# Optimization experiments

Hardware: AMD Instinct MI355X
Metric: run time of the kernel (lower is better)

## Reference

```python
import jax, jax.numpy as jnp
import numpy as np

B, S, H = 2, 1024, 1024
E, I, K = 16, 512, 4
SHARED_I = 512 * 2  # moe_intermediate_size * moe_num_shared_experts
NORM_MIN = 1e-12


def _mlp(x, gw, uw, dw):
    # gated SiLU MLP: down(silu(gate(x)) * up(x))
    return (jax.nn.silu(x @ gw) * (x @ uw)) @ dw


def setup_inputs() -> dict:
    key = jax.random.key(0)
    ks = jax.random.split(key, 9)
    s = 0.02
    return {
        "hidden_states": jax.random.normal(ks[0], (B, S, H), jnp.float32),
        "gate_weight": jax.random.normal(ks[1], (H, E), jnp.float32) * s,
        "corr_bias": jnp.zeros((E,), jnp.float32),
        "gate_w": jax.random.normal(ks[2], (E, H, I), jnp.float32) * s,
        "up_w": jax.random.normal(ks[3], (E, H, I), jnp.float32) * s,
        "down_w": jax.random.normal(ks[4], (E, I, H), jnp.float32) * s,
        "shared_gate_w": jax.random.normal(ks[5], (H, SHARED_I), jnp.float32) * s,
        "shared_up_w": jax.random.normal(ks[6], (H, SHARED_I), jnp.float32) * s,
        "shared_down_w": jax.random.normal(ks[7], (SHARED_I, H), jnp.float32) * s,
    }


def reference(hidden_states, gate_weight, corr_bias, gate_w, up_w, down_w,
              shared_gate_w, shared_up_w, shared_down_w):
    b, s, h = hidden_states.shape
    x = hidden_states.reshape(-1, h)                      # [T, H]
    T = x.shape[0]

    # shared experts (full-capacity, always applied)
    shared_out = _mlp(x, shared_gate_w, shared_up_w, shared_down_w)

    # router in float32
    router_logits = x.astype(jnp.float32) @ gate_weight   # [T, E]
    probs = jax.nn.softmax(router_logits, axis=-1)
    # top-k on bias-corrected scores, weights gathered from uncorrected probs
    _, selected = jax.lax.top_k(probs + corr_bias[None, :], K)  # [T, K]
    rw = jnp.take_along_axis(probs, selected, axis=-1)          # [T, K]
    rw = rw / jnp.maximum(rw.sum(-1, keepdims=True), NORM_MIN)
    rw = rw.astype(x.dtype)

    # dense combine weights [T, E] (zero for unselected experts)
    cw = jnp.zeros((T, gate_weight.shape[1]), x.dtype)
    cw = cw.at[jnp.arange(T)[:, None], selected].add(rw)

    # grouped expert MLPs (full capacity, no token dropping)
    g = jnp.einsum('th,ehi->tei', x, gate_w)
    u = jnp.einsum('th,ehi->tei', x, up_w)
    eo = jnp.einsum('tei,eih->teh', jax.nn.silu(g) * u, down_w)
    final = jnp.einsum('teh,te->th', eo, cw) + shared_out

    return final.reshape(b, s, h), router_logits
```

## Files before the change

kernel.cpp:

```cpp
#include <hip/hip_runtime.h>
#include <hip/hip_bf16.h>

#define T_TOK 2048
#define H_DIM 1024
#define E_NUM 16
#define I_DIM 512
#define K_TOP 4
#define SI_DIM 1024

typedef __bf16 bf16x8 __attribute__((ext_vector_type(8)));
typedef __bf16 bf16x4 __attribute__((ext_vector_type(4)));
typedef float f32x4 __attribute__((ext_vector_type(4)));

#define GL2L(g, l)                                                                       \
  __builtin_amdgcn_global_load_lds((const __attribute__((address_space(1))) void*)(g),   \
                                   (__attribute__((address_space(3))) void*)(l), 16, 0, 0)
#define BAR() __builtin_amdgcn_s_barrier()

__global__ __launch_bounds__(256) void transpose_all_kernel(
    const float* __restrict__ gate_w, const float* __restrict__ up_w,
    const float* __restrict__ down_w, const float* __restrict__ sgw,
    const float* __restrict__ suw, const float* __restrict__ sdw,
    const float* __restrict__ gate_weight, __bf16* __restrict__ gw_t,
    __bf16* __restrict__ uw_t, __bf16* __restrict__ dw_t, __bf16* __restrict__ sgw_t,
    __bf16* __restrict__ suw_t, __bf16* __restrict__ sdw_t, float* __restrict__ gwt_f) {
  int tid = threadIdx.x;
  if (blockIdx.x >= 6912) {
    int b = blockIdx.x - 6912;
#pragma unroll
    for (int k = 0; k < 4; k++) {
      int idx = k * 4096 + b * 256 + tid;
      gwt_f[idx] = gate_weight[(idx & 1023) * E_NUM + (idx >> 10)];
    }
    return;
  }
  __shared__ __align__(16) __bf16 tile[64 * 64];
  int t = blockIdx.x;
  const float* in;
  __bf16* out;
  int R, C, r0, c0;
  if (t < 4096) {
    bool g = t < 2048;
    int b = t & 2047;
    int z = b >> 7;
    int ti = b & 127;
    R = H_DIM;
    C = I_DIM;
    r0 = (ti >> 3) * 64;
    c0 = (ti & 7) * 64;
    size_t off = (size_t)z * R * C;
    in = (g ? gate_w : up_w) + off;
    out = (g ? gw_t : uw_t) + off;
  } else if (t < 6144) {
    int b = t - 4096;
    int z = b >> 7;
    int ti = b & 127;
    R = I_DIM;
    C = H_DIM;
    r0 = (ti >> 4) * 64;
    c0 = (ti & 15) * 64;
    size_t off = (size_t)z * R * C;
    in = down_w + off;
    out = dw_t + off;
  } else {
    int b = t - 6144;
    int m = b >> 8;
    int ti = b & 255;
    R = 1024;
    C = 1024;
    r0 = (ti >> 4) * 64;
    c0 = (ti & 15) * 64;
    in = m == 0 ? sgw : m == 1 ? suw : sdw;
    out = m == 0 ? sgw_t : m == 1 ? suw_t : sdw_t;
  }
#pragma unroll
  for (int q = 0; q < 2; q++) {
    int lin8 = q * 256 + tid;
    int row = lin8 >> 3, cb = lin8 & 7;
    const float* ip = in + (size_t)(r0 + row) * C + c0 + cb * 8;
    float4 v0 = *(const float4*)ip;
    float4 v1 = *(const float4*)(ip + 4);
    bf16x8 o;
    o[0] = (__bf16)v0.x; o[1] = (__bf16)v0.y; o[2] = (__bf16)v0.z; o[3] = (__bf16)v0.w;
    o[4] = (__bf16)v1.x; o[5] = (__bf16)v1.y; o[6] = (__bf16)v1.z; o[7] = (__bf16)v1.w;
    int pcb = cb ^ ((row >> 3) & 7);
    *(bf16x8*)&tile[row * 64 + pcb * 8] = o;
  }
  __syncthreads();
  int p = tid >> 3, seg = tid & 7;
  int c = p * 2;
  const unsigned int* ldsw = (const unsigned int*)tile;
  unsigned int d[8];
#pragma unroll
  for (int i = 0; i < 8; i++) {
    int r = seg * 8 + i;
    int pcb = (p >> 2) ^ seg;
    d[i] = ldsw[r * 32 + pcb * 4 + (p & 3)];
  }
  unsigned int lo[4], hi[4];
#pragma unroll
  for (int j = 0; j < 4; j++) {
    lo[j] = __builtin_amdgcn_perm(d[2 * j + 1], d[2 * j], 0x05040100u);
    hi[j] = __builtin_amdgcn_perm(d[2 * j + 1], d[2 * j], 0x07060302u);
  }
  __bf16* op0 = out + (size_t)(c0 + c) * R + r0 + seg * 8;
  __bf16* op1 = op0 + R;
  *(uint4*)op0 = make_uint4(lo[0], lo[1], lo[2], lo[3]);
  *(uint4*)op1 = make_uint4(hi[0], hi[1], hi[2], hi[3]);
}

__global__ __launch_bounds__(256) void router_kernel(
    const float* __restrict__ x, const float* __restrict__ gwt, const float* __restrict__ cbias,
    float* __restrict__ logits_out, __bf16* __restrict__ x_bf, int* __restrict__ selE,
    float* __restrict__ selW) {
  int t = blockIdx.x;
  int tid = threadIdx.x;
  int wid = tid >> 6, lane = tid & 63;
  int e = lane >> 2, cl = lane & 3;
  int c = wid * 4 + cl;
  const float* xr = x + (size_t)t * H_DIM + c * 64;
  const float* gr = gwt + (size_t)e * H_DIM + c * 64;
  float a0 = 0.f, a1 = 0.f, a2 = 0.f, a3 = 0.f;
#pragma unroll
  for (int j = 0; j < 16; j++) {
    float4 xv = *(const float4*)(xr + j * 4);
    float4 gv = *(const float4*)(gr + j * 4);
    if (e == 0) {
      bf16x4 o = {(__bf16)xv.x, (__bf16)xv.y, (__bf16)xv.z, (__bf16)xv.w};
      *(bf16x4*)(x_bf + (size_t)t * H_DIM + c * 64 + j * 4) = o;
    }
    a0 = fmaf(xv.x, gv.x, a0);
    a1 = fmaf(xv.y, gv.y, a1);
    a2 = fmaf(xv.z, gv.z, a2);
    a3 = fmaf(xv.w, gv.w, a3);
  }
  float a = (a0 + a1) + (a2 + a3);
  a += __shfl_xor(a, 1);
  a += __shfl_xor(a, 2);
  __shared__ float part[4][16];
  if (cl == 0) part[wid][e] = a;
  __syncthreads();
  if (wid != 0) return;
  float logit = -1e30f;
  if (lane < E_NUM)
    logit = (part[0][lane] + part[1][lane]) + (part[2][lane] + part[3][lane]);
  if (lane < E_NUM) logits_out[(size_t)t * E_NUM + lane] = logit;
  float m = logit;
#pragma unroll
  for (int mk = 8; mk >= 1; mk >>= 1) m = fmaxf(m, __shfl_xor(m, mk));
  float p = __expf(logit - m);
  float s = p;
#pragma unroll
  for (int mk = 8; mk >= 1; mk >>= 1) s += __shfl_xor(s, mk);
  p /= s;
  float score = (lane < E_NUM) ? p + cbias[lane] : -1e30f;
  int sel[K_TOP];
  float w[K_TOP];
#pragma unroll
  for (int k = 0; k < K_TOP; k++) {
    float bv = score;
    int bi = (lane < E_NUM) ? lane : 999;
#pragma unroll
    for (int mk = 1; mk <= 8; mk <<= 1) {
      float ov = __shfl_xor(bv, mk);
      int oi = __shfl_xor(bi, mk);
      if (ov > bv || (ov == bv && oi < bi)) {
        bv = ov;
        bi = oi;
      }
    }
    sel[k] = bi;
    w[k] = __shfl(p, bi);
    if (lane == bi) score = -1e30f;
  }
  if (lane == 0) {
    float wsum = fmaxf(w[0] + w[1] + w[2] + w[3], 1e-12f);
#pragma unroll
    for (int k = 0; k < K_TOP; k++) {
      selE[t * K_TOP + k] = sel[k];
      selW[t * K_TOP + k] = w[k] / wsum;
    }
  }
}

__global__ __launch_bounds__(1024) void count_place_kernel(
    const int* __restrict__ selE, int* __restrict__ counts, int* __restrict__ offs,
    int* __restrict__ slot_of_tk, int* __restrict__ tok_of_slot) {
  int tid = threadIdx.x;
  int wv = tid >> 6, lane = tid & 63;
  unsigned long long lt = (1ULL << lane) - 1ULL;
  __shared__ int wcnt[16][16];
  __shared__ int wbase[16][16];
  __shared__ int glob[16];
  __shared__ int offsh[16];
  if (tid < 16) glob[tid] = 0;
  __syncthreads();
  int ex[8], rk[8];
#pragma unroll
  for (int r = 0; r < 8; r++) {
    int e = selE[r * 1024 + tid];
    ex[r] = e;
    int rank = 0;
#pragma unroll
    for (int q = 0; q < 16; q++) {
      unsigned long long b = __ballot(e == q);
      int c = __popcll(b & lt);
      if (e == q) rank = c;
      if (lane == q) wcnt[wv][q] = __popcll(b);
    }
    __syncthreads();
    if (wv == 0 && lane < 16) {
      int run = glob[lane];
#pragma unroll
      for (int w = 0; w < 16; w++) {
        wbase[w][lane] = run;
        run += wcnt[w][lane];
      }
      glob[lane] = run;
    }
    __syncthreads();
    rk[r] = rank + wbase[wv][e];
    __syncthreads();
  }
  if (wv == 0 && lane == 0) {
    int s = 0;
#pragma unroll
    for (int q = 0; q < 16; q++) {
      offsh[q] = s;
      s += glob[q];
    }
  }
  __syncthreads();
  if (tid < 16) {
    counts[tid] = glob[tid];
    offs[tid] = offsh[tid];
  }
#pragma unroll
  for (int r = 0; r < 8; r++) {
    int entry = r * 1024 + tid;
    int slot = offsh[ex[r]] + rk[r];
    slot_of_tk[entry] = slot;
    tok_of_slot[slot] = entry >> 2;
  }
}

__global__ __launch_bounds__(256, 3) void gemm_stage1(
    const __bf16* __restrict__ x_bf, const int* __restrict__ tok_of_slot,
    const int* __restrict__ counts, const int* __restrict__ offs, const __bf16* __restrict__ gw_t,
    const __bf16* __restrict__ uw_t, const __bf16* __restrict__ sgw_t,
    const __bf16* __restrict__ suw_t, __bf16* __restrict__ he, __bf16* __restrict__ hs) {
  __shared__ __align__(16) __bf16 Alds[128 * 64];
  __shared__ __align__(16) __bf16 Bgl[2 * 64 * 64];
  __shared__ __align__(16) __bf16 Bul[2 * 64 * 64];
  int z = blockIdx.z, bx = blockIdx.x, m0 = blockIdx.y * 128;
  const __bf16 *Bg, *Bu;
  __bf16* Cp;
  const int* tokIdx;
  int rowOff, M, ldC, n0;
  if (z < E_NUM) {
    M = counts[z];
    if (m0 >= M) return;
    tokIdx = tok_of_slot;
    rowOff = offs[z];
    Bg = gw_t + (size_t)z * I_DIM * H_DIM;
    Bu = uw_t + (size_t)z * I_DIM * H_DIM;
    Cp = he;
    ldC = I_DIM;
    n0 = bx * 64;
  } else {
    tokIdx = nullptr;
    rowOff = 0;
    M = T_TOK;
    Bg = sgw_t;
    Bu = suw_t;
    Cp = hs;
    ldC = SI_DIM;
    n0 = (z - E_NUM) * 512 + bx * 64;
  }
  int tid = threadIdx.x;
  int wave = tid >> 6, lane = tid & 63;
  int rsub = lane >> 3, chunk = lane & 7;
  int sch = (chunk ^ rsub) * 8;
  size_t aB[4], bB[2];
#pragma unroll
  for (int j = 0; j < 4; j++) {
    int r = wave * 32 + j * 8 + rsub;
    int ar = m0 + r;
    ar = ar < M - 1 ? ar : M - 1;
    int grow = tokIdx ? tokIdx[rowOff + ar] : rowOff + ar;
    aB[j] = (size_t)grow * H_DIM + sch;
  }
#pragma unroll
  for (int j = 0; j < 2; j++) {
    int r = wave * 16 + j * 8 + rsub;
    bB[j] = (size_t)(n0 + r) * H_DIM + sch;
  }
  int wm = (wave >> 1) * 64, wn = (wave & 1) * 32;
  int rl = lane & 15, gq = lane >> 4;
  int xa = rl & 7;

  auto STAGE_A = [&](int k0) {
#pragma unroll
    for (int j = 0; j < 4; j++) GL2L(x_bf + aB[j] + k0, Alds + (wave * 32 + j * 8) * 64);
  };
  auto STAGE_B = [&](int k0, int buf) {
#pragma unroll
    for (int j = 0; j < 2; j++) {
      int ld = buf * 4096 + (wave * 16 + j * 8) * 64;
      GL2L(Bg + bB[j] + k0, Bgl + ld);
      GL2L(Bu + bB[j] + k0, Bul + ld);
    }
  };

  f32x4 accg[4][2] = {}, accu[4][2] = {};
  const int NT = H_DIM / 64;
  STAGE_A(0);
  STAGE_B(0, 0);
  int buf = 0;
  for (int t = 0; t < NT; ++t) {
    if (t + 1 < NT) {
      STAGE_B((t + 1) << 6, buf ^ 1);
      asm volatile("s_waitcnt vmcnt(4)" ::: "memory");
    } else {
      asm volatile("s_waitcnt vmcnt(0)" ::: "memory");
    }
    BAR();
    const __bf16* Bgr = Bgl + buf * 4096;
    const __bf16* Bur = Bul + buf * 4096;
#pragma unroll
    for (int s = 0; s < 2; s++) {
      int lc = ((s * 4 + gq) ^ xa) * 8;
      bf16x8 af[4], bg[2], bu[2];
#pragma unroll
      for (int m = 0; m < 4; m++) af[m] = *(const bf16x8*)&Alds[(wm + m * 16 + rl) * 64 + lc];
#pragma unroll
      for (int n = 0; n < 2; n++) {
        bg[n] = *(const bf16x8*)&Bgr[(wn + n * 16 + rl) * 64 + lc];
        bu[n] = *(const bf16x8*)&Bur[(wn + n * 16 + rl) * 64 + lc];
      }
#pragma unroll
      for (int m = 0; m < 4; m++)
#pragma unroll
        for (int n = 0; n < 2; n++) {
          accg[m][n] =
              __builtin_amdgcn_mfma_f32_16x16x32_bf16(af[m], bg[n], accg[m][n], 0, 0, 0);
          accu[m][n] =
              __builtin_amdgcn_mfma_f32_16x16x32_bf16(af[m], bu[n], accu[m][n], 0, 0, 0);
        }
    }
    BAR();
    if (t + 1 < NT) STAGE_A((t + 1) << 6);
    buf ^= 1;
  }
#pragma unroll
  for (int m = 0; m < 4; m++) {
#pragma unroll
    for (int b = 0; b < 4; b++) {
      int row = m0 + wm + m * 16 + gq * 4 + b;
      if (row < M) {
        size_t rb = (size_t)(rowOff + row) * ldC + n0 + wn + rl;
#pragma unroll
        for (int n = 0; n < 2; n++) {
          float g = accg[m][n][b];
          float u = accu[m][n][b];
          float h = g / (1.f + __expf(-g)) * u;
          Cp[rb + n * 16] = (__bf16)h;
        }
      }
    }
  }
}

__global__ __launch_bounds__(256, 4) void gemm_stage2(
    const __bf16* __restrict__ he, const __bf16* __restrict__ hs, const int* __restrict__ counts,
    const int* __restrict__ offs, const __bf16* __restrict__ dw_t,
    const __bf16* __restrict__ sdw_t, __bf16* __restrict__ eo, __bf16* __restrict__ so) {
  __shared__ __align__(16) __bf16 Alds[64 * 64];
  __shared__ __align__(16) __bf16 Blds[2 * 64 * 64];
  int z = blockIdx.z, bx = blockIdx.x, m0 = blockIdx.y * 64;
  const __bf16 *A, *Bp;
  __bf16* Cp;
  int rowOff, M, K;
  if (z < E_NUM) {
    M = counts[z];
    if (m0 >= M) return;
    A = he;
    rowOff = offs[z];
    K = I_DIM;
    Bp = dw_t + (size_t)z * H_DIM * I_DIM;
    Cp = eo;
  } else {
    A = hs;
    rowOff = 0;
    M = T_TOK;
    K = SI_DIM;
    Bp = sdw_t;
    Cp = so;
  }
  int n0 = bx * 64;
  int tid = threadIdx.x;
  int wave = tid >> 6, lane = tid & 63;
  int rsub = lane >> 3, chunk = lane & 7;
  int sch = (chunk ^ rsub) * 8;
  size_t aB[2], bB[2];
#pragma unroll
  for (int j = 0; j < 2; j++) {
    int r = wave * 16 + j * 8 + rsub;
    int ar = m0 + r;
    ar = ar < M - 1 ? ar : M - 1;
    aB[j] = (size_t)(rowOff + ar) * K + sch;
    bB[j] = (size_t)(n0 + r) * K + sch;
  }
  int wm = (wave >> 1) * 32, wn = (wave & 1) * 32;
  int rl = lane & 15, gq = lane >> 4;
  int xa = rl & 7;

  auto STAGE_A = [&](int k0) {
#pragma unroll
    for (int j = 0; j < 2; j++) GL2L(A + aB[j] + k0, Alds + (wave * 16 + j * 8) * 64);
  };
  auto STAGE_B = [&](int k0, int b) {
#pragma unroll
    for (int j = 0; j < 2; j++)
      GL2L(Bp + bB[j] + k0, Blds + b * 4096 + (wave * 16 + j * 8) * 64);
  };

  f32x4 acc[2][2] = {};
  const int NT = K >> 6;
  STAGE_A(0);
  STAGE_B(0, 0);
  int buf = 0;
  for (int t = 0; t < NT; ++t) {
    if (t + 1 < NT) {
      STAGE_B((t + 1) << 6, buf ^ 1);
      asm volatile("s_waitcnt vmcnt(2)" ::: "memory");
    } else {
      asm volatile("s_waitcnt vmcnt(0)" ::: "memory");
    }
    BAR();
    const __bf16* Br = Blds + buf * 4096;
#pragma unroll
    for (int s = 0; s < 2; s++) {
      int lc = ((s * 4 + gq) ^ xa) * 8;
      bf16x8 af[2], bfr[2];
#pragma unroll
      for (int m = 0; m < 2; m++) af[m] = *(const bf16x8*)&Alds[(wm + m * 16 + rl) * 64 + lc];
#pragma unroll
      for (int n = 0; n < 2; n++) bfr[n] = *(const bf16x8*)&Br[(wn + n * 16 + rl) * 64 + lc];
#pragma unroll
      for (int m = 0; m < 2; m++)
#pragma unroll
        for (int n = 0; n < 2; n++)
          acc[m][n] =
              __builtin_amdgcn_mfma_f32_16x16x32_bf16(af[m], bfr[n], acc[m][n], 0, 0, 0);
    }
    BAR();
    if (t + 1 < NT) STAGE_A((t + 1) << 6);
    buf ^= 1;
  }
#pragma unroll
  for (int m = 0; m < 2; m++) {
#pragma unroll
    for (int b = 0; b < 4; b++) {
      int row = m0 + wm + m * 16 + gq * 4 + b;
      if (row < M) {
        size_t rb = (size_t)(rowOff + row) * H_DIM + n0 + wn + rl;
#pragma unroll
        for (int n = 0; n < 2; n++) Cp[rb + n * 16] = (__bf16)acc[m][n][b];
      }
    }
  }
}

__global__ void combine_kernel(const __bf16* __restrict__ eo, const __bf16* __restrict__ so,
                               const int* __restrict__ slot_of_tk, const float* __restrict__ selW,
                               float* __restrict__ out) {
  int idx = blockIdx.x * blockDim.x + threadIdx.x;
  int t = idx >> 8;
  int h4 = (idx & 255) * 4;
  if (t >= T_TOK) return;
  bf16x4 sv = *(const bf16x4*)(so + (size_t)t * H_DIM + h4);
  float a0 = (float)sv[0], a1 = (float)sv[1], a2 = (float)sv[2], a3 = (float)sv[3];
#pragma unroll
  for (int k = 0; k < K_TOP; k++) {
    int slot = slot_of_tk[t * K_TOP + k];
    float w = selW[t * K_TOP + k];
    bf16x4 ev = *(const bf16x4*)(eo + (size_t)slot * H_DIM + h4);
    a0 += w * (float)ev[0];
    a1 += w * (float)ev[1];
    a2 += w * (float)ev[2];
    a3 += w * (float)ev[3];
  }
  *(float4*)(out + (size_t)t * H_DIM + h4) = make_float4(a0, a1, a2, a3);
}

extern "C" void kernel_launch(void* const* d_in, const int* in_sizes, int n_in, void* d_out,
                              int out_size, void* d_ws, size_t ws_size, hipStream_t stream) {
  const float* x = (const float*)d_in[0];
  const float* gate_weight = (const float*)d_in[1];
  const float* corr_bias = (const float*)d_in[2];
  const float* gate_w = (const float*)d_in[3];
  const float* up_w = (const float*)d_in[4];
  const float* down_w = (const float*)d_in[5];
  const float* sgw = (const float*)d_in[6];
  const float* suw = (const float*)d_in[7];
  const float* sdw = (const float*)d_in[8];
  float* out = (float*)d_out;
  float* logits_out = out + (size_t)T_TOK * H_DIM;

  char* wsb = (char*)d_ws;
  size_t o = 0;
  auto nxt = [&](size_t bytes) -> void* {
    void* p = wsb + o;
    o += (bytes + 1023) & ~(size_t)1023;
    return p;
  };
  const size_t EXP_ELE = (size_t)T_TOK * K_TOP * I_DIM;
  const size_t SH_ELE = (size_t)T_TOK * SI_DIM;
  __bf16* x_bf = (__bf16*)nxt((size_t)T_TOK * H_DIM * 2);
  __bf16* gw_t = (__bf16*)nxt((size_t)E_NUM * I_DIM * H_DIM * 2);
  __bf16* uw_t = (__bf16*)nxt((size_t)E_NUM * I_DIM * H_DIM * 2);
  __bf16* dw_t = (__bf16*)nxt((size_t)E_NUM * H_DIM * I_DIM * 2);
  __bf16* sgw_t = (__bf16*)nxt((size_t)SI_DIM * H_DIM * 2);
  __bf16* suw_t = (__bf16*)nxt((size_t)SI_DIM * H_DIM * 2);
  __bf16* sdw_t = (__bf16*)nxt((size_t)H_DIM * SI_DIM * 2);
  __bf16* h_all = (__bf16*)nxt((EXP_ELE + SH_ELE) * 2);
  __bf16* eo = (__bf16*)nxt((size_t)T_TOK * K_TOP * H_DIM * 2);
  __bf16* so = (__bf16*)nxt((size_t)T_TOK * H_DIM * 2);
  float* gwt_f = (float*)nxt((size_t)E_NUM * H_DIM * 4);
  int* counts = (int*)nxt(64);
  int* offs = (int*)nxt(128);
  int* selE = (int*)nxt((size_t)T_TOK * K_TOP * 4);
  float* selW = (float*)nxt((size_t)T_TOK * K_TOP * 4);
  int* slot_of_tk = (int*)nxt((size_t)T_TOK * K_TOP * 4);
  int* tok_of_slot = (int*)nxt((size_t)T_TOK * K_TOP * 4);
  __bf16* he = h_all;
  __bf16* hs = h_all + EXP_ELE;
  (void)ws_size;
  (void)in_sizes;
  (void)n_in;
  (void)out_size;

  transpose_all_kernel<<<6928, 256, 0, stream>>>(gate_w, up_w, down_w, sgw, suw, sdw,
                                                 gate_weight, gw_t, uw_t, dw_t, sgw_t, suw_t,
                                                 sdw_t, gwt_f);
  router_kernel<<<T_TOK, 256, 0, stream>>>(x, gwt_f, corr_bias, logits_out, x_bf, selE, selW);
  count_place_kernel<<<1, 1024, 0, stream>>>(selE, counts, offs, slot_of_tk, tok_of_slot);

  gemm_stage1<<<dim3(8, 16, E_NUM + 2), 256, 0, stream>>>(x_bf, tok_of_slot, counts, offs, gw_t,
                                                          uw_t, sgw_t, suw_t, he, hs);
  gemm_stage2<<<dim3(16, 32, E_NUM + 1), 256, 0, stream>>>(he, hs, counts, offs, dw_t, sdw_t, eo,
                                                           so);

  combine_kernel<<<(T_TOK * H_DIM / 4) / 256, 256, 0, stream>>>(eo, so, slot_of_tk, selW, out);
}
```

Measured before the change: 154.6 us.

## Restructure router so each wavefront handles two tokens without LDS reduction

The router kernel now assigns two tokens to each wavefront and eight tokens to each block. Each lane covers one expert over a quarter of the hidden dimension, and partial sums are reduced with cross-lane shuffles, which removes the shared-memory partial buffer and the block barrier. The intent is to cut block count, barrier cost and idle waves in the softmax/top-k tail. In exchange, each lane runs a longer serial loop with strided per-lane loads that coalesce less well, and there are only 256 blocks to cover the GPU.

New measurement: 160.7 us. +4.0%, slower.

```diff
diff --git a/kernel.cpp b/kernel.cpp
--- a/kernel.cpp
+++ b/kernel.cpp
@@ -113,72 +113,68 @@
     const float* __restrict__ x, const float* __restrict__ gwt, const float* __restrict__ cbias,
     float* __restrict__ logits_out, __bf16* __restrict__ x_bf, int* __restrict__ selE,
     float* __restrict__ selW) {
-  int t = blockIdx.x;
   int tid = threadIdx.x;
   int wid = tid >> 6, lane = tid & 63;
-  int e = lane >> 2, cl = lane & 3;
-  int c = wid * 4 + cl;
-  const float* xr = x + (size_t)t * H_DIM + c * 64;
-  const float* gr = gwt + (size_t)e * H_DIM + c * 64;
-  float a0 = 0.f, a1 = 0.f, a2 = 0.f, a3 = 0.f;
-#pragma unroll
-  for (int j = 0; j < 16; j++) {
-    float4 xv = *(const float4*)(xr + j * 4);
-    float4 gv = *(const float4*)(gr + j * 4);
-    if (e == 0) {
-      bf16x4 o = {(__bf16)xv.x, (__bf16)xv.y, (__bf16)xv.z, (__bf16)xv.w};
-      *(bf16x4*)(x_bf + (size_t)t * H_DIM + c * 64 + j * 4) = o;
-    }
-    a0 = fmaf(xv.x, gv.x, a0);
-    a1 = fmaf(xv.y, gv.y, a1);
-    a2 = fmaf(xv.z, gv.z, a2);
-    a3 = fmaf(xv.w, gv.w, a3);
-  }
-  float a = (a0 + a1) + (a2 + a3);
-  a += __shfl_xor(a, 1);
-  a += __shfl_xor(a, 2);
-  __shared__ float part[4][16];
-  if (cl == 0) part[wid][e] = a;
-  __syncthreads();
-  if (wid != 0) return;
-  float logit = -1e30f;
-  if (lane < E_NUM)
-    logit = (part[0][lane] + part[1][lane]) + (part[2][lane] + part[3][lane]);
-  if (lane < E_NUM) logits_out[(size_t)t * E_NUM + lane] = logit;
-  float m = logit;
-#pragma unroll
-  for (int mk = 8; mk >= 1; mk >>= 1) m = fmaxf(m, __shfl_xor(m, mk));
-  float p = __expf(logit - m);
-  float s = p;
-#pragma unroll
-  for (int mk = 8; mk >= 1; mk >>= 1) s += __shfl_xor(s, mk);
-  p /= s;
-  float score = (lane < E_NUM) ? p + cbias[lane] : -1e30f;
-  int sel[K_TOP];
-  float w[K_TOP];
-#pragma unroll
-  for (int k = 0; k < K_TOP; k++) {
-    float bv = score;
-    int bi = (lane < E_NUM) ? lane : 999;
-#pragma unroll
-    for (int mk = 1; mk <= 8; mk <<= 1) {
-      float ov = __shfl_xor(bv, mk);
-      int oi = __shfl_xor(bi, mk);
-      if (ov > bv || (ov == bv && oi < bi)) {
-        bv = ov;
-        bi = oi;
-      }
-    }
-    sel[k] = bi;
-    w[k] = __shfl(p, bi);
-    if (lane == bi) score = -1e30f;
-  }
-  if (lane == 0) {
-    float wsum = fmaxf(w[0] + w[1] + w[2] + w[3], 1e-12f);
+  int e = lane & 15, h = lane >> 4;
+  float bias = cbias[e];
+#pragma unroll
+  for (int tt = 0; tt < 2; tt++) {
+    int t = blockIdx.x * 8 + wid * 2 + tt;
+    const float* xr = x + (size_t)t * H_DIM + h * 256;
+    const float* gr = gwt + (size_t)e * H_DIM + h * 256;
+    float a0 = 0.f, a1 = 0.f, a2 = 0.f, a3 = 0.f;
+#pragma unroll
+    for (int j = 0; j < 64; j++) {
+      float4 xv = *(const float4*)(xr + j * 4);
+      float4 gv = *(const float4*)(gr + j * 4);
+      if (e == 0) {
+        bf16x4 o = {(__bf16)xv.x, (__bf16)xv.y, (__bf16)xv.z, (__bf16)xv.w};
+        *(bf16x4*)(x_bf + (size_t)t * H_DIM + h * 256 + j * 4) = o;
+      }
+      a0 = fmaf(xv.x, gv.x, a0);
+      a1 = fmaf(xv.y, gv.y, a1);
+      a2 = fmaf(xv.z, gv.z, a2);
+      a3 = fmaf(xv.w, gv.w, a3);
+    }
+    float a = (a0 + a1) + (a2 + a3);
+    a += __shfl_xor(a, 16);
+    a += __shfl_xor(a, 32);
+    if (lane < E_NUM) logits_out[(size_t)t * E_NUM + lane] = a;
+    float m = a;
+#pragma unroll
+    for (int mk = 8; mk >= 1; mk >>= 1) m = fmaxf(m, __shfl_xor(m, mk));
+    float p = __expf(a - m);
+    float s = p;
+#pragma unroll
+    for (int mk = 8; mk >= 1; mk >>= 1) s += __shfl_xor(s, mk);
+    p /= s;
+    float score = p + bias;
+    int sel[K_TOP];
+    float w[K_TOP];
 #pragma unroll
     for (int k = 0; k < K_TOP; k++) {
-      selE[t * K_TOP + k] = sel[k];
-      selW[t * K_TOP + k] = w[k] / wsum;
+      float bv = score;
+      int bi = e;
+#pragma unroll
+      for (int mk = 1; mk <= 8; mk <<= 1) {
+        float ov = __shfl_xor(bv, mk);
+        int oi = __shfl_xor(bi, mk);
+        if (ov > bv || (ov == bv && oi < bi)) {
+          bv = ov;
+          bi = oi;
+        }
+      }
+      sel[k] = bi;
+      w[k] = __shfl(p, bi);
+      if (e == bi) score = -1e30f;
+    }
+    if (lane == 0) {
+      float wsum = fmaxf(w[0] + w[1] + w[2] + w[3], 1e-12f);
+#pragma unroll
+      for (int k = 0; k < K_TOP; k++) {
+        selE[t * K_TOP + k] = sel[k];
+        selW[t * K_TOP + k] = w[k] / wsum;
+      }
     }
   }
 }
@@ -544,7 +540,8 @@
   transpose_all_kernel<<<6928, 256, 0, stream>>>(gate_w, up_w, down_w, sgw, suw, sdw,
                                                  gate_weight, gw_t, uw_t, dw_t, sgw_t, suw_t,
                                                  sdw_t, gwt_f);
-  router_kernel<<<T_TOK, 256, 0, stream>>>(x, gwt_f, corr_bias, logits_out, x_bf, selE, selW);
+  router_kernel<<<T_TOK / 8, 256, 0, stream>>>(x, gwt_f, corr_bias, logits_out, x_bf, selE,
+                                               selW);
   count_place_kernel<<<1, 1024, 0, stream>>>(selE, counts, offs, slot_of_tk, tok_of_slot);
 
   gemm_stage1<<<dim3(8, 16, E_NUM + 2), 256, 0, stream>>>(x_bf, tok_of_slot, counts, offs, gw_t,
```
